# Performance work log

Measured on AMD Instinct MI355X. Metric: run time of the kernel, lower is better.

## Reference

```python
import jax, jax.numpy as jnp
import numpy as np
from jax import lax

VOCAB = 50000   # marker token id == vocab_size
EMB = 1024
HID = 1024      # bidirectional total
HD = HID // 2   # per-direction hidden
LAYERS = 2
B, T = 32, 512


def setup_inputs() -> dict:
    key = jax.random.key(0)
    ks = jax.random.split(key, 12)
    seq = jax.random.randint(ks[0], (B, T), 1, VOCAB)
    pos = jax.random.randint(ks[1], (B,), 0, T)
    seq = seq.at[jnp.arange(B), pos].set(VOCAB)  # exactly one marker per row
    label = (jax.random.uniform(ks[2], (B,)) > 0.5).astype(jnp.float32)
    s = 1.0 / np.sqrt(HD)
    w_emb = jax.random.normal(ks[3], (VOCAB + 1, EMB), jnp.float32) * 0.05
    w_ih = jax.random.uniform(ks[4], (LAYERS, 2, 4 * HD, EMB), jnp.float32, -s, s)
    w_hh = jax.random.uniform(ks[5], (LAYERS, 2, 4 * HD, HD), jnp.float32, -s, s)
    b = jax.random.uniform(ks[6], (LAYERS, 2, 4 * HD), jnp.float32, -s, s)
    w1 = jax.random.normal(ks[7], (HD, HID), jnp.float32) * 0.03
    b1 = jnp.zeros((HD,), jnp.float32)
    w2 = jax.random.normal(ks[8], (1, HD), jnp.float32) * 0.03
    b2 = jnp.zeros((1,), jnp.float32)
    return {"seq": seq, "label": label, "w_emb": w_emb, "w_ih": w_ih,
            "w_hh": w_hh, "b": b, "w1": w1, "b1": b1, "w2": w2, "b2": b2}


def _run_dir(x, Wih, Whh, bb, reverse):
    # x: [B,T,In]; precompute input contribution to all 4 gates (i,f,g,o order, torch layout)
    gx = jnp.einsum('bti,gi->btg', x, Wih) + bb  # [B,T,4*HD]

    def step(carry, g):
        h, c = carry
        g = g + h @ Whh.T
        i, f, gg, o = jnp.split(g, 4, axis=-1)
        c = jax.nn.sigmoid(f) * c + jax.nn.sigmoid(i) * jnp.tanh(gg)
        h = jax.nn.sigmoid(o) * jnp.tanh(c)
        return (h, c), h

    h0 = jnp.zeros((x.shape[0], HD), x.dtype)
    _, hs = lax.scan(step, (h0, h0), gx.transpose(1, 0, 2), reverse=reverse)
    return hs.transpose(1, 0, 2)  # [B,T,HD], time order preserved


def reference(seq, label, w_emb, w_ih, w_hh, b, w1, b1, w2, b2):
    emb = w_emb.at[0].set(0.0)[seq]  # padding_idx=0 -> zero vector
    x = emb
    for l in range(LAYERS):
        fwd = _run_dir(x, w_ih[l, 0], w_hh[l, 0], b[l, 0], False)
        bwd = _run_dir(x, w_ih[l, 1], w_hh[l, 1], b[l, 1], True)
        x = jnp.concatenate([fwd, bwd], axis=-1)  # [B,T,HID]
    # masked_select at the single marker position per row -> [B,HID]
    idx = jnp.argmax(seq == VOCAB, axis=1)
    hidden = x[jnp.arange(x.shape[0]), idx]
    h = jnp.tanh(hidden @ w1.T + b1)
    logit = (h @ w2.T + b2)[:, 0]
    # BCEWithLogits, mean reduction: softplus(z) - z*y
    return jnp.mean(jax.nn.softplus(logit) - logit * label)
```

## Files before the change

kernel.cpp:

```cpp
#include <hip/hip_runtime.h>
#include <stdint.h>

typedef unsigned short u16;
typedef __bf16 bf16x8 __attribute__((ext_vector_type(8)));
typedef float  f32x4  __attribute__((ext_vector_type(4)));

#define GPTR(p) ((const __attribute__((address_space(1))) void*)(p))
#define LPTR(p) ((__attribute__((address_space(3))) void*)(p))

__device__ __forceinline__ u16 f2bf(float f) {
  uint32_t u = __float_as_uint(f);
  u += 0x7FFFu + ((u >> 16) & 1u);
  return (u16)(u >> 16);
}
__device__ __forceinline__ float bf2f(u16 h) {
  return __uint_as_float(((uint32_t)h) << 16);
}
__device__ __forceinline__ float sigf(float x) { return 1.0f / (1.0f + __expf(-x)); }
__device__ __forceinline__ float tanhf_(float x) { return 1.0f - 2.0f / (__expf(2.0f * x) + 1.0f); }

__global__ void k_emb(const int* __restrict__ seq, const float* __restrict__ wemb,
                      u16* __restrict__ x1) {
  const int row = blockIdx.x;
  const int tok = seq[row];
  float4 v = ((const float4*)(wemb + (size_t)tok * 1024))[threadIdx.x];
  uint32_t lo = (uint32_t)f2bf(v.x) | ((uint32_t)f2bf(v.y) << 16);
  uint32_t hi = (uint32_t)f2bf(v.z) | ((uint32_t)f2bf(v.w) << 16);
  *(uint2*)(x1 + (size_t)row * 1024 + threadIdx.x * 4) = make_uint2(lo, hi);
}

__global__ void k_idx(const int* __restrict__ seq, int* __restrict__ idxb) {
  const int tid = threadIdx.x;
  const int b = tid >> 3, part = tid & 7;
  for (int t = part * 64; t < part * 64 + 64; ++t)
    if (seq[b * 512 + t] == 50000) idxb[b] = t;
}

__global__ void k_cast(const float* __restrict__ src, u16* __restrict__ dst) {
  const int i = blockIdx.x * 256 + threadIdx.x;
  float4 v = ((const float4*)src)[i];
  uint32_t lo = (uint32_t)f2bf(v.x) | ((uint32_t)f2bf(v.y) << 16);
  uint32_t hi = (uint32_t)f2bf(v.z) | ((uint32_t)f2bf(v.w) << 16);
  *(uint2*)(dst + (size_t)i * 4) = make_uint2(lo, hi);
}

__global__ __launch_bounds__(256) void k_gemm(
    const u16* __restrict__ X, const u16* __restrict__ W,
    const float* __restrict__ bias, u16* __restrict__ gx)
{
  __shared__ u16 As[128 * 64];
  __shared__ u16 Bs[128 * 64];
  const int tid = threadIdx.x;
  const int lane = tid & 63;
  const int wv = tid >> 6;
  const int wm = wv >> 1, wn = wv & 1;
  const int bm = blockIdx.x, bn = blockIdx.y;
  const u16* Xb = X + (size_t)bm * 128 * 1024;
  const u16* Wb = W + (size_t)bn * 128 * 1024;
  const int srow_in = lane >> 3;
  const int sg      = (lane & 7) ^ srow_in;
  f32x4 acc[4][4] = {};
  for (int k0 = 0; k0 < 1024; k0 += 64) {
    #pragma unroll
    for (int n = 0; n < 4; ++n) {
      const int c = n * 4 + wv;
      const int r = c * 8 + srow_in;
      __builtin_amdgcn_global_load_lds(GPTR(Xb + (size_t)r * 1024 + k0 + sg * 8),
                                       LPTR(&As[c * 512 + lane * 8]), 16, 0, 0);
      __builtin_amdgcn_global_load_lds(GPTR(Wb + (size_t)r * 1024 + k0 + sg * 8),
                                       LPTR(&Bs[c * 512 + lane * 8]), 16, 0, 0);
    }
    __syncthreads();
    const int kq0 = lane >> 4;
    bf16x8 a4[4][2], b4[4][2];
    #pragma unroll
    for (int mt = 0; mt < 4; ++mt) {
      const int ra = wm * 64 + mt * 16 + (lane & 15);
      #pragma unroll
      for (int h = 0; h < 2; ++h)
        a4[mt][h] = *(const bf16x8*)&As[ra * 64 + (((kq0 + h * 4) ^ (ra & 7)) * 8)];
    }
    #pragma unroll
    for (int nt = 0; nt < 4; ++nt) {
      const int rb = wn * 64 + nt * 16 + (lane & 15);
      #pragma unroll
      for (int h = 0; h < 2; ++h)
        b4[nt][h] = *(const bf16x8*)&Bs[rb * 64 + (((kq0 + h * 4) ^ (rb & 7)) * 8)];
    }
    #pragma unroll
    for (int mt = 0; mt < 4; ++mt)
      #pragma unroll
      for (int nt = 0; nt < 4; ++nt) {
        acc[mt][nt] = __builtin_amdgcn_mfma_f32_16x16x32_bf16(a4[mt][0], b4[nt][0], acc[mt][nt], 0, 0, 0);
        acc[mt][nt] = __builtin_amdgcn_mfma_f32_16x16x32_bf16(a4[mt][1], b4[nt][1], acc[mt][nt], 0, 0, 0);
      }
    __syncthreads();
  }
  #pragma unroll
  for (int mt = 0; mt < 4; ++mt) {
    const int mbase = bm * 128 + wm * 64 + mt * 16 + ((lane >> 4) << 2);
    #pragma unroll
    for (int nt = 0; nt < 4; ++nt) {
      const int n = bn * 128 + wn * 64 + nt * 16 + (lane & 15);
      const float bi = bias[n];
      const int d = n >> 11;
      const int nn = n & 2047;
      const int q = nn >> 9;
      const int j = nn & 511;
      const int col = (j >> 4) * 64 + q * 16 + (j & 15);
      #pragma unroll
      for (int r = 0; r < 4; ++r) {
        const int mm = mbase + r;
        const int b = mm >> 9, t = mm & 511;
        gx[((size_t)(d * 512 + t) * 32 + b) * 2048 + col] = f2bf(acc[mt][nt][r] + bi);
      }
    }
  }
}

__global__ __launch_bounds__(256, 1) void k_rec(
    const u16* __restrict__ gx, const float* __restrict__ whh,
    u16* __restrict__ xout, u16* hstep)
{
  const int bid = blockIdx.x;
  const int dir = bid >> 5;
  const int db = bid & 31;
  const int j0 = db * 16;
  const int tid = threadIdx.x;
  const int lane = tid & 63;
  const int wv = tid >> 6;
  const int mh = wv >> 1, nh = wv & 1;
  const int R = lane & 15;
  const int ks = lane >> 4;

  __shared__ float G[2][32][68];

  bf16x8 bw[2][16];
  {
    #pragma unroll
    for (int nt = 0; nt < 2; ++nt) {
      const int q = nh * 2 + nt;
      const float* wp = whh + ((size_t)dir * 2048 + q * 512 + j0 + R) * 512 + ks * 8;
      #pragma unroll
      for (int kt = 0; kt < 16; ++kt) {
        float4 v0 = *(const float4*)(wp + kt * 32);
        float4 v1 = *(const float4*)(wp + kt * 32 + 4);
        union { u16 u[8]; bf16x8 v; } t;
        t.u[0] = f2bf(v0.x); t.u[1] = f2bf(v0.y); t.u[2] = f2bf(v0.z); t.u[3] = f2bf(v0.w);
        t.u[4] = f2bf(v1.x); t.u[5] = f2bf(v1.y); t.u[6] = f2bf(v1.z); t.u[7] = f2bf(v1.w);
        bw[nt][kt] = t.v;
      }
    }
  }

  const int eb = tid >> 3;
  const int pr = (tid & 7) * 2;
  float c0 = 0.f, c1 = 0.f;

  const size_t dirbase = (size_t)dir * 512 * 16384;
  const u16* apbase = hstep + dirbase + (size_t)(ks >> 1) * 512 + (mh * 16 + R) * 16 + (ks & 1) * 8;
  const u16* prbase = hstep + dirbase + (size_t)(lane & 31) * 512 + 510;
  const u16* gxeb   = gx + ((size_t)dir * 512 * 32 + eb) * 2048 + db * 64 + pr;

  uint32_t gq[4];
  {
    const int t0 = dir ? 511 : 0;
    const uint32_t* g0 = (const uint32_t*)(gxeb + (size_t)t0 * 65536);
    gq[0] = g0[0]; gq[1] = g0[8]; gq[2] = g0[16]; gq[3] = g0[24];
  }

  for (int s = 0; s < 512; ++s) {
    const int tcur = dir ? (511 - s) : s;
    const int gb = s & 1;
    f32x4 acc0 = {0.f,0.f,0.f,0.f}, acc1 = {0.f,0.f,0.f,0.f};

    if (s) {
      const size_t slot = (size_t)(s - 1) * 16384;
      const u16* ap = apbase + slot;
      __builtin_amdgcn_s_sleep(16);
      {
        const u16* pp = prbase + slot;
        while (true) {
          uint32_t fv;
          asm volatile("global_load_dword %0, %1, off sc0 sc1\n\ts_waitcnt vmcnt(0)"
                       : "=v"(fv) : "v"(pp) : "memory");
          if (__all((int)(fv != 0xFFFFFFFFu))) break;
        }
      }
      __builtin_amdgcn_sched_barrier(0);
      uint4 afu[16];
      #pragma unroll
      for (int kt = 0; kt < 16; ++kt)
        asm volatile("global_load_dwordx4 %0, %1, off sc0 sc1"
                     : "=v"(afu[kt]) : "v"(ap + kt * 1024) : "memory");
      asm volatile("s_waitcnt vmcnt(8)" ::: "memory");
      __builtin_amdgcn_sched_barrier(0);
      while (true) {
        unsigned mask = 0;
        #pragma unroll
        for (int kt = 0; kt < 8; ++kt) {
          int ok = (afu[kt].x != 0xFFFFFFFFu) && (afu[kt].y != 0xFFFFFFFFu) &&
                   (afu[kt].z != 0xFFFFFFFFu) && (afu[kt].w != 0xFFFFFFFFu);
          if (!__all(ok)) mask |= 1u << kt;
        }
        if (!mask) break;
        #pragma unroll
        for (int kt = 0; kt < 8; ++kt)
          if (mask & (1u << kt))
            asm volatile("global_load_dwordx4 %0, %1, off sc0 sc1"
                         : "=v"(afu[kt]) : "v"(ap + kt * 1024) : "memory");
        asm volatile("s_waitcnt vmcnt(0)" ::: "memory");
        __builtin_amdgcn_sched_barrier(0);
      }
      f32x4 a0 = {0.f,0.f,0.f,0.f}, a1 = {0.f,0.f,0.f,0.f};
      f32x4 b0 = {0.f,0.f,0.f,0.f}, b1 = {0.f,0.f,0.f,0.f};
      #pragma unroll
      for (int kt = 0; kt < 8; kt += 2) {
        bf16x8 x = __builtin_bit_cast(bf16x8, afu[kt]);
        bf16x8 y = __builtin_bit_cast(bf16x8, afu[kt + 1]);
        a0 = __builtin_amdgcn_mfma_f32_16x16x32_bf16(x, bw[0][kt],     a0, 0, 0, 0);
        a1 = __builtin_amdgcn_mfma_f32_16x16x32_bf16(x, bw[1][kt],     a1, 0, 0, 0);
        b0 = __builtin_amdgcn_mfma_f32_16x16x32_bf16(y, bw[0][kt + 1], b0, 0, 0, 0);
        b1 = __builtin_amdgcn_mfma_f32_16x16x32_bf16(y, bw[1][kt + 1], b1, 0, 0, 0);
      }
      asm volatile("s_waitcnt vmcnt(0)" ::: "memory");
      __builtin_amdgcn_sched_barrier(0);
      while (true) {
        unsigned mask = 0;
        #pragma unroll
        for (int kt = 8; kt < 16; ++kt) {
          int ok = (afu[kt].x != 0xFFFFFFFFu) && (afu[kt].y != 0xFFFFFFFFu) &&
                   (afu[kt].z != 0xFFFFFFFFu) && (afu[kt].w != 0xFFFFFFFFu);
          if (!__all(ok)) mask |= 1u << (kt - 8);
        }
        if (!mask) break;
        #pragma unroll
        for (int kt = 8; kt < 16; ++kt)
          if (mask & (1u << (kt - 8)))
            asm volatile("global_load_dwordx4 %0, %1, off sc0 sc1"
                         : "=v"(afu[kt]) : "v"(ap + kt * 1024) : "memory");
        asm volatile("s_waitcnt vmcnt(0)" ::: "memory");
        __builtin_amdgcn_sched_barrier(0);
      }
      #pragma unroll
      for (int kt = 8; kt < 16; kt += 2) {
        bf16x8 x = __builtin_bit_cast(bf16x8, afu[kt]);
        bf16x8 y = __builtin_bit_cast(bf16x8, afu[kt + 1]);
        a0 = __builtin_amdgcn_mfma_f32_16x16x32_bf16(x, bw[0][kt],     a0, 0, 0, 0);
        a1 = __builtin_amdgcn_mfma_f32_16x16x32_bf16(x, bw[1][kt],     a1, 0, 0, 0);
        b0 = __builtin_amdgcn_mfma_f32_16x16x32_bf16(y, bw[0][kt + 1], b0, 0, 0, 0);
        b1 = __builtin_amdgcn_mfma_f32_16x16x32_bf16(y, bw[1][kt + 1], b1, 0, 0, 0);
      }
      acc0 = a0 + b0;
      acc1 = a1 + b1;
    }

    #pragma unroll
    for (int r = 0; r < 4; ++r) {
      G[gb][mh * 16 + (lane >> 4) * 4 + r][nh * 32 + (lane & 15)]      = acc0[r];
      G[gb][mh * 16 + (lane >> 4) * 4 + r][nh * 32 + 16 + (lane & 15)] = acc1[r];
    }
    __syncthreads();

    {
      float i0 = G[gb][eb][pr]      + bf2f((u16)(gq[0] & 0xFFFF));
      float i1 = G[gb][eb][pr + 1]  + bf2f((u16)(gq[0] >> 16));
      float f0 = G[gb][eb][pr + 16] + bf2f((u16)(gq[1] & 0xFFFF));
      float f1 = G[gb][eb][pr + 17] + bf2f((u16)(gq[1] >> 16));
      float g0 = G[gb][eb][pr + 32] + bf2f((u16)(gq[2] & 0xFFFF));
      float g1 = G[gb][eb][pr + 33] + bf2f((u16)(gq[2] >> 16));
      float o0 = G[gb][eb][pr + 48] + bf2f((u16)(gq[3] & 0xFFFF));
      float o1 = G[gb][eb][pr + 49] + bf2f((u16)(gq[3] >> 16));
      c0 = sigf(f0) * c0 + sigf(i0) * tanhf_(g0);
      c1 = sigf(f1) * c1 + sigf(i1) * tanhf_(g1);
      float h0 = sigf(o0) * tanhf_(c0);
      float h1 = sigf(o1) * tanhf_(c1);
      uint32_t hp = (uint32_t)f2bf(h0) | ((uint32_t)f2bf(h1) << 16);
      u16* hdst = hstep + dirbase + (size_t)s * 16384 + (size_t)db * 512 + eb * 16 + pr;
      asm volatile("global_store_dword %0, %1, off sc0 sc1"
                   :: "v"(hdst), "v"(hp) : "memory");
      *(uint32_t*)(xout + ((size_t)eb * 512 + tcur) * 1024 + dir * 512 + j0 + pr) = hp;
    }
    if (s < 511) {
      const int tn = dir ? (511 - (s + 1)) : (s + 1);
      const uint32_t* gn = (const uint32_t*)(gxeb + (size_t)tn * 65536);
      gq[0] = gn[0]; gq[1] = gn[8]; gq[2] = gn[16]; gq[3] = gn[24];
    }
  }
}

__global__ void k_cls1(const u16* __restrict__ x3, const int* __restrict__ idxb,
                       const float* __restrict__ w1, const float* __restrict__ b1,
                       float* __restrict__ h1) {
  __shared__ u16 hid[32][1024];
  const int tid = threadIdx.x;
  for (int g = tid; g < 4096; g += 256) {
    const int b = g >> 7;
    const int c8 = (g & 127) * 8;
    *(uint4*)&hid[b][c8] = *(const uint4*)(x3 + ((size_t)b * 512 + idxb[b]) * 1024 + c8);
  }
  __syncthreads();
  for (int p = tid; p < 1024; p += 256) {
    const int j = blockIdx.x * 32 + (p >> 5);
    const int b = p & 31;
    const float4* wr = (const float4*)(w1 + (size_t)j * 1024);
    float s = 0.f;
    for (int k4 = 0; k4 < 256; ++k4) {
      float4 wv = wr[k4];
      const int k = k4 * 4;
      s += bf2f(hid[b][k]) * wv.x + bf2f(hid[b][k + 1]) * wv.y
         + bf2f(hid[b][k + 2]) * wv.z + bf2f(hid[b][k + 3]) * wv.w;
    }
    h1[b * 512 + j] = tanhf_(s + b1[j]);
  }
}

__global__ void k_cls2(const float* __restrict__ h1, const float* __restrict__ w2,
                       const float* __restrict__ b2, const float* __restrict__ label,
                       float* __restrict__ out) {
  const int lane = threadIdx.x;
  float loss = 0.f;
  for (int b = 0; b < 32; ++b) {
    float s = 0.f;
    for (int k = lane; k < 512; k += 64) s += h1[b * 512 + k] * w2[k];
    for (int off = 32; off; off >>= 1) s += __shfl_down(s, off);
    if (lane == 0) {
      const float z = s + b2[0];
      const float y = label[b];
      const float sp = fmaxf(z, 0.f) + log1pf(__expf(-fabsf(z)));
      loss += sp - z * y;
    }
  }
  if (lane == 0) out[0] = loss / 32.0f;
}

extern "C" void kernel_launch(void* const* d_in, const int* in_sizes, int n_in,
                              void* d_out, int out_size, void* d_ws, size_t ws_size,
                              hipStream_t stream) {
  const int*   seq   = (const int*)  d_in[0];
  const float* label = (const float*)d_in[1];
  const float* wemb  = (const float*)d_in[2];
  const float* wih   = (const float*)d_in[3];
  const float* whh   = (const float*)d_in[4];
  const float* bb    = (const float*)d_in[5];
  const float* w1    = (const float*)d_in[6];
  const float* b1    = (const float*)d_in[7];
  const float* w2    = (const float*)d_in[8];
  const float* b2    = (const float*)d_in[9];

  u16* x1   = (u16*)d_ws;
  u16* x2   = x1 + (size_t)16777216;
  u16* gxb  = x2 + (size_t)16777216;
  u16* wb   = gxb + (size_t)67108864;
  float* h1 = (float*)(wb + 4194304);
  int* idxb = (int*)(h1 + 16384);

  k_emb<<<16384, 256, 0, stream>>>(seq, wemb, x1);
  k_idx<<<1, 256, 0, stream>>>(seq, idxb);
  k_cast<<<4096, 256, 0, stream>>>(wih, wb);
  k_gemm<<<dim3(128, 32), 256, 0, stream>>>(x1, wb, bb, gxb);
  hipMemsetAsync(x1, 0xFF, (size_t)33554432, stream);
  k_rec<<<64, 256, 0, stream>>>(gxb, whh, x2, x1);
  k_cast<<<4096, 256, 0, stream>>>(wih + 4194304, wb);
  k_gemm<<<dim3(128, 32), 256, 0, stream>>>(x2, wb, bb + 4096, gxb);
  hipMemsetAsync(x2, 0xFF, (size_t)33554432, stream);
  k_rec<<<64, 256, 0, stream>>>(gxb, whh + 2097152, x1, x2);
  k_cls1<<<16, 256, 0, stream>>>(x1, idxb, w1, b1, h1);
  k_cls2<<<1, 64, 0, stream>>>(h1, w2, b2, label, (float*)d_out);
}
```

Baseline: 4.000 ms.

## Fuse input-projection GEMM with LSTM recurrence via sentinel-polled streaming

Merges the input-gate GEMM and the recurrent LSTM kernel into one launch. The first 64 blocks run the recurrence, and the rest compute GEMM tiles ordered alternately from both time ends. Activations switch to a time-major layout so each GEMM tile covers contiguous timesteps, and gx is pre-filled with a 0xFFFF sentinel. Recurrence blocks spin with coherent loads until their gates are valid, which hides most of the GEMM behind the serial recurrence. The cost is two extra large memsets per layer, a bigger workspace requirement with a fallback path, and spin-wait and deadlock risk if the GEMM blocks cannot be scheduled.

```diff
diff --git a/kernel.cpp b/kernel.cpp
--- a/kernel.cpp
+++ b/kernel.cpp
@@ -7,6 +7,7 @@
 
 #define GPTR(p) ((const __attribute__((address_space(1))) void*)(p))
 #define LPTR(p) ((__attribute__((address_space(3))) void*)(p))
+#define GVALID(X) (int)((((X) & 0xFFFFu) != 0xFFFFu) & (((X) >> 16) != 0xFFFFu))
 
 __device__ __forceinline__ u16 f2bf(float f) {
   uint32_t u = __float_as_uint(f);
@@ -23,10 +24,11 @@
                       u16* __restrict__ x1) {
   const int row = blockIdx.x;
   const int tok = seq[row];
+  const int b = row >> 9, t = row & 511;
   float4 v = ((const float4*)(wemb + (size_t)tok * 1024))[threadIdx.x];
   uint32_t lo = (uint32_t)f2bf(v.x) | ((uint32_t)f2bf(v.y) << 16);
   uint32_t hi = (uint32_t)f2bf(v.z) | ((uint32_t)f2bf(v.w) << 16);
-  *(uint2*)(x1 + (size_t)row * 1024 + threadIdx.x * 4) = make_uint2(lo, hi);
+  *(uint2*)(x1 + ((size_t)t * 32 + b) * 1024 + threadIdx.x * 4) = make_uint2(lo, hi);
 }
 
 __global__ void k_idx(const int* __restrict__ seq, int* __restrict__ idxb) {
@@ -44,96 +46,99 @@
   *(uint2*)(dst + (size_t)i * 4) = make_uint2(lo, hi);
 }
 
-__global__ __launch_bounds__(256) void k_gemm(
+__global__ __launch_bounds__(256, 1) void k_fused(
+    const int rec_blocks,
     const u16* __restrict__ X, const u16* __restrict__ W,
-    const float* __restrict__ bias, u16* __restrict__ gx)
+    const float* __restrict__ bias, u16* __restrict__ gx,
+    const float* __restrict__ whh, u16* __restrict__ xout, u16* hstep)
 {
-  __shared__ u16 As[128 * 64];
-  __shared__ u16 Bs[128 * 64];
+  __shared__ u16 smem[16384];
   const int tid = threadIdx.x;
-  const int lane = tid & 63;
-  const int wv = tid >> 6;
-  const int wm = wv >> 1, wn = wv & 1;
-  const int bm = blockIdx.x, bn = blockIdx.y;
-  const u16* Xb = X + (size_t)bm * 128 * 1024;
-  const u16* Wb = W + (size_t)bn * 128 * 1024;
-  const int srow_in = lane >> 3;
-  const int sg      = (lane & 7) ^ srow_in;
-  f32x4 acc[4][4] = {};
-  for (int k0 = 0; k0 < 1024; k0 += 64) {
-    #pragma unroll
-    for (int n = 0; n < 4; ++n) {
-      const int c = n * 4 + wv;
-      const int r = c * 8 + srow_in;
-      __builtin_amdgcn_global_load_lds(GPTR(Xb + (size_t)r * 1024 + k0 + sg * 8),
-                                       LPTR(&As[c * 512 + lane * 8]), 16, 0, 0);
-      __builtin_amdgcn_global_load_lds(GPTR(Wb + (size_t)r * 1024 + k0 + sg * 8),
-                                       LPTR(&Bs[c * 512 + lane * 8]), 16, 0, 0);
-    }
-    __syncthreads();
-    const int kq0 = lane >> 4;
-    bf16x8 a4[4][2], b4[4][2];
+
+  if ((int)blockIdx.x >= rec_blocks) {
+    u16* As = smem;
+    u16* Bs = smem + 8192;
+    const int bk = blockIdx.x - rec_blocks;
+    const int bn = bk & 31;
+    const int bmo = bk >> 5;
+    const int bm = (bmo & 1) ? (127 - (bmo >> 1)) : (bmo >> 1);
+    const int lane = tid & 63;
+    const int wv = tid >> 6;
+    const int wm = wv >> 1, wn = wv & 1;
+    const u16* Xb = X + (size_t)bm * 128 * 1024;
+    const u16* Wb = W + (size_t)bn * 128 * 1024;
+    const int srow_in = lane >> 3;
+    const int sg      = (lane & 7) ^ srow_in;
+    f32x4 acc[4][4] = {};
+    for (int k0 = 0; k0 < 1024; k0 += 64) {
+      #pragma unroll
+      for (int n = 0; n < 4; ++n) {
+        const int c = n * 4 + wv;
+        const int r = c * 8 + srow_in;
+        __builtin_amdgcn_global_load_lds(GPTR(Xb + (size_t)r * 1024 + k0 + sg * 8),
+                                         LPTR(&As[c * 512 + lane * 8]), 16, 0, 0);
+        __builtin_amdgcn_global_load_lds(GPTR(Wb + (size_t)r * 1024 + k0 + sg * 8),
+                                         LPTR(&Bs[c * 512 + lane * 8]), 16, 0, 0);
+      }
+      __syncthreads();
+      const int kq0 = lane >> 4;
+      bf16x8 a4[4][2], b4[4][2];
+      #pragma unroll
+      for (int mt = 0; mt < 4; ++mt) {
+        const int ra = wm * 64 + mt * 16 + (lane & 15);
+        #pragma unroll
+        for (int h = 0; h < 2; ++h)
+          a4[mt][h] = *(const bf16x8*)&As[ra * 64 + (((kq0 + h * 4) ^ (ra & 7)) * 8)];
+      }
+      #pragma unroll
+      for (int nt = 0; nt < 4; ++nt) {
+        const int rb = wn * 64 + nt * 16 + (lane & 15);
+        #pragma unroll
+        for (int h = 0; h < 2; ++h)
+          b4[nt][h] = *(const bf16x8*)&Bs[rb * 64 + (((kq0 + h * 4) ^ (rb & 7)) * 8)];
+      }
+      #pragma unroll
+      for (int mt = 0; mt < 4; ++mt)
+        #pragma unroll
+        for (int nt = 0; nt < 4; ++nt) {
+          acc[mt][nt] = __builtin_amdgcn_mfma_f32_16x16x32_bf16(a4[mt][0], b4[nt][0], acc[mt][nt], 0, 0, 0);
+          acc[mt][nt] = __builtin_amdgcn_mfma_f32_16x16x32_bf16(a4[mt][1], b4[nt][1], acc[mt][nt], 0, 0, 0);
+        }
+      __syncthreads();
+    }
     #pragma unroll
     for (int mt = 0; mt < 4; ++mt) {
-      const int ra = wm * 64 + mt * 16 + (lane & 15);
-      #pragma unroll
-      for (int h = 0; h < 2; ++h)
-        a4[mt][h] = *(const bf16x8*)&As[ra * 64 + (((kq0 + h * 4) ^ (ra & 7)) * 8)];
-    }
-    #pragma unroll
-    for (int nt = 0; nt < 4; ++nt) {
-      const int rb = wn * 64 + nt * 16 + (lane & 15);
-      #pragma unroll
-      for (int h = 0; h < 2; ++h)
-        b4[nt][h] = *(const bf16x8*)&Bs[rb * 64 + (((kq0 + h * 4) ^ (rb & 7)) * 8)];
-    }
-    #pragma unroll
-    for (int mt = 0; mt < 4; ++mt)
+      const int mbase = bm * 128 + wm * 64 + mt * 16 + ((lane >> 4) << 2);
       #pragma unroll
       for (int nt = 0; nt < 4; ++nt) {
-        acc[mt][nt] = __builtin_amdgcn_mfma_f32_16x16x32_bf16(a4[mt][0], b4[nt][0], acc[mt][nt], 0, 0, 0);
-        acc[mt][nt] = __builtin_amdgcn_mfma_f32_16x16x32_bf16(a4[mt][1], b4[nt][1], acc[mt][nt], 0, 0, 0);
-      }
-    __syncthreads();
-  }
-  #pragma unroll
-  for (int mt = 0; mt < 4; ++mt) {
-    const int mbase = bm * 128 + wm * 64 + mt * 16 + ((lane >> 4) << 2);
-    #pragma unroll
-    for (int nt = 0; nt < 4; ++nt) {
-      const int n = bn * 128 + wn * 64 + nt * 16 + (lane & 15);
-      const float bi = bias[n];
-      const int d = n >> 11;
-      const int nn = n & 2047;
-      const int q = nn >> 9;
-      const int j = nn & 511;
-      const int col = (j >> 4) * 64 + q * 16 + (j & 15);
-      #pragma unroll
-      for (int r = 0; r < 4; ++r) {
-        const int mm = mbase + r;
-        const int b = mm >> 9, t = mm & 511;
-        gx[((size_t)(d * 512 + t) * 32 + b) * 2048 + col] = f2bf(acc[mt][nt][r] + bi);
-      }
-    }
-  }
-}
-
-__global__ __launch_bounds__(256, 1) void k_rec(
-    const u16* __restrict__ gx, const float* __restrict__ whh,
-    u16* __restrict__ xout, u16* hstep)
-{
+        const int n = bn * 128 + wn * 64 + nt * 16 + (lane & 15);
+        const float bi = bias[n];
+        const int d = n >> 11;
+        const int nn = n & 2047;
+        const int q = nn >> 9;
+        const int j = nn & 511;
+        const int col = (j >> 4) * 64 + q * 16 + (j & 15);
+        #pragma unroll
+        for (int r = 0; r < 4; ++r) {
+          const int mm = mbase + r;
+          const int t = mm >> 5, b = mm & 31;
+          gx[((size_t)(d * 512 + t) * 32 + b) * 2048 + col] = f2bf(acc[mt][nt][r] + bi);
+        }
+      }
+    }
+    return;
+  }
+
+  float (*G)[32][68] = (float(*)[32][68])smem;
   const int bid = blockIdx.x;
   const int dir = bid >> 5;
   const int db = bid & 31;
   const int j0 = db * 16;
-  const int tid = threadIdx.x;
   const int lane = tid & 63;
   const int wv = tid >> 6;
   const int mh = wv >> 1, nh = wv & 1;
   const int R = lane & 15;
   const int ks = lane >> 4;
-
-  __shared__ float G[2][32][68];
 
   bf16x8 bw[2][16];
   {
@@ -261,6 +266,23 @@
       G[gb][mh * 16 + (lane >> 4) * 4 + r][nh * 32 + 16 + (lane & 15)] = acc1[r];
     }
     __syncthreads();
+
+    {
+      int ok = GVALID(gq[0]) & GVALID(gq[1]) & GVALID(gq[2]) & GVALID(gq[3]);
+      if (!__all(ok)) {
+        const u16* gp = gxeb + (size_t)tcur * 65536;
+        while (true) {
+          asm volatile("global_load_dword %0, %1, off sc0 sc1" : "=v"(gq[0]) : "v"(gp +  0) : "memory");
+          asm volatile("global_load_dword %0, %1, off sc0 sc1" : "=v"(gq[1]) : "v"(gp + 16) : "memory");
+          asm volatile("global_load_dword %0, %1, off sc0 sc1" : "=v"(gq[2]) : "v"(gp + 32) : "memory");
+          asm volatile("global_load_dword %0, %1, off sc0 sc1" : "=v"(gq[3]) : "v"(gp + 48) : "memory");
+          asm volatile("s_waitcnt vmcnt(0)" ::: "memory");
+          __builtin_amdgcn_sched_barrier(0);
+          ok = GVALID(gq[0]) & GVALID(gq[1]) & GVALID(gq[2]) & GVALID(gq[3]);
+          if (__all(ok)) break;
+        }
+      }
+    }
 
     {
       float i0 = G[gb][eb][pr]      + bf2f((u16)(gq[0] & 0xFFFF));
@@ -279,7 +301,7 @@
       u16* hdst = hstep + dirbase + (size_t)s * 16384 + (size_t)db * 512 + eb * 16 + pr;
       asm volatile("global_store_dword %0, %1, off sc0 sc1"
                    :: "v"(hdst), "v"(hp) : "memory");
-      *(uint32_t*)(xout + ((size_t)eb * 512 + tcur) * 1024 + dir * 512 + j0 + pr) = hp;
+      *(uint32_t*)(xout + ((size_t)tcur * 32 + eb) * 1024 + dir * 512 + j0 + pr) = hp;
     }
     if (s < 511) {
       const int tn = dir ? (511 - (s + 1)) : (s + 1);
@@ -297,7 +319,7 @@
   for (int g = tid; g < 4096; g += 256) {
     const int b = g >> 7;
     const int c8 = (g & 127) * 8;
-    *(uint4*)&hid[b][c8] = *(const uint4*)(x3 + ((size_t)b * 512 + idxb[b]) * 1024 + c8);
+    *(uint4*)&hid[b][c8] = *(const uint4*)(x3 + ((size_t)idxb[b] * 32 + b) * 1024 + c8);
   }
   __syncthreads();
   for (int p = tid; p < 1024; p += 256) {
@@ -351,20 +373,35 @@
   u16* x1   = (u16*)d_ws;
   u16* x2   = x1 + (size_t)16777216;
   u16* gxb  = x2 + (size_t)16777216;
-  u16* wb   = gxb + (size_t)67108864;
-  float* h1 = (float*)(wb + 4194304);
+  u16* wb1  = gxb + (size_t)67108864;
+  float* h1 = (float*)(wb1 + 4194304);
   int* idxb = (int*)(h1 + 16384);
+  u16* wb2  = (u16*)(idxb + 32);
+  u16* hs   = wb2 + (size_t)4194304;
+  const size_t need = (size_t)((char*)(hs + 16777216) - (char*)d_ws);
+  const bool fused = ws_size >= need;
 
   k_emb<<<16384, 256, 0, stream>>>(seq, wemb, x1);
   k_idx<<<1, 256, 0, stream>>>(seq, idxb);
-  k_cast<<<4096, 256, 0, stream>>>(wih, wb);
-  k_gemm<<<dim3(128, 32), 256, 0, stream>>>(x1, wb, bb, gxb);
-  hipMemsetAsync(x1, 0xFF, (size_t)33554432, stream);
-  k_rec<<<64, 256, 0, stream>>>(gxb, whh, x2, x1);
-  k_cast<<<4096, 256, 0, stream>>>(wih + 4194304, wb);
-  k_gemm<<<dim3(128, 32), 256, 0, stream>>>(x2, wb, bb + 4096, gxb);
-  hipMemsetAsync(x2, 0xFF, (size_t)33554432, stream);
-  k_rec<<<64, 256, 0, stream>>>(gxb, whh + 2097152, x1, x2);
+  k_cast<<<4096, 256, 0, stream>>>(wih, wb1);
+
+  if (fused) {
+    k_cast<<<4096, 256, 0, stream>>>(wih + 4194304, wb2);
+    hipMemsetAsync(gxb, 0xFF, (size_t)134217728, stream);
+    hipMemsetAsync(hs, 0xFF, (size_t)33554432, stream);
+    k_fused<<<64 + 4096, 256, 0, stream>>>(64, x1, wb1, bb, gxb, whh, x2, hs);
+    hipMemsetAsync(gxb, 0xFF, (size_t)134217728, stream);
+    hipMemsetAsync(hs, 0xFF, (size_t)33554432, stream);
+    k_fused<<<64 + 4096, 256, 0, stream>>>(64, x2, wb2, bb + 4096, gxb, whh + 2097152, x1, hs);
+  } else {
+    k_fused<<<4096, 256, 0, stream>>>(0, x1, wb1, bb, gxb, whh, x2, x1);
+    hipMemsetAsync(x1, 0xFF, (size_t)33554432, stream);
+    k_fused<<<64, 256, 0, stream>>>(64, x1, wb1, bb, gxb, whh, x2, x1);
+    k_cast<<<4096, 256, 0, stream>>>(wih + 4194304, wb1);
+    k_fused<<<4096, 256, 0, stream>>>(0, x2, wb1, bb + 4096, gxb, whh + 2097152, x1, x2);
+    hipMemsetAsync(x2, 0xFF, (size_t)33554432, stream);
+    k_fused<<<64, 256, 0, stream>>>(64, x2, wb1, bb + 4096, gxb, whh + 2097152, x1, x2);
+  }
   k_cls1<<<16, 256, 0, stream>>>(x1, idxb, w1, b1, h1);
   k_cls2<<<1, 64, 0, stream>>>(h1, w2, b2, label, (float*)d_out);
 }
```

Measured after the change: 3.781 ms. 5.5% less time.
